# Kernel optimization log

Hardware: AMD Instinct MI355X
Metric: run time of the kernel (lower is better)

The kernel has to match this reference:

```python
import jax, jax.numpy as jnp
import numpy as np
from math import sqrt

DIM = 2048
N_HEADS = 2
HEAD_DIM = DIM // N_HEADS  # 1024 == RoPE dims (dim // 2)
ROPE_DIMS = DIM // 2
ROPE_BASE = 10000.0


def apply_rope(x, dims=ROPE_DIMS, base=ROPE_BASE, offset=0):
    # x: [B, H, L, Dh]; non-traditional (split-half) RoPE over sequence axis
    L = x.shape[-2]
    pos = jnp.arange(offset, offset + L, dtype=x.dtype)[:, None]          # [L,1]
    inv = jnp.exp(jnp.arange(0, dims, 2, dtype=x.dtype) * (-np.log(base) / dims))  # [dims//2]
    theta = pos * inv                                                      # [L, dims//2]
    cos, sin = jnp.cos(theta), jnp.sin(theta)
    h = dims // 2
    x1, x2 = x[..., :h], x[..., h:dims]
    rx1 = x1 * cos - x2 * sin
    rx2 = x1 * sin + x2 * cos
    if dims < x.shape[-1]:
        return jnp.concatenate([rx1, rx2, x[..., dims:]], axis=-1)
    return jnp.concatenate([rx1, rx2], axis=-1)


def setup_inputs() -> dict:
    key = jax.random.key(0)
    ks = jax.random.split(key, 6)
    B, L = 4, 2048
    x = jax.random.normal(ks[0], (B, L, DIM), dtype=jnp.float32)
    # causal additive mask
    causal = jnp.tril(jnp.ones((L, L), dtype=bool))
    mask = jnp.where(causal, 0.0, -1e9).astype(jnp.float32)
    s1 = 1.0 / sqrt(DIM)
    Wqkv_w = jax.random.normal(ks[1], (3 * DIM, DIM), dtype=jnp.float32) * s1
    Wqkv_b = jnp.zeros((3 * DIM,), dtype=jnp.float32)
    out_w = jax.random.normal(ks[2], (DIM, DIM), dtype=jnp.float32) * s1
    out_b = jnp.zeros((DIM,), dtype=jnp.float32)
    return {"x": x, "mask": mask, "Wqkv_w": Wqkv_w, "Wqkv_b": Wqkv_b,
            "out_w": out_w, "out_b": out_b}


def reference(x, mask, Wqkv_w, Wqkv_b, out_w, out_b):
    B, L, D = x.shape
    H, Dh = N_HEADS, HEAD_DIM
    qkv = x @ Wqkv_w.T + Wqkv_b                       # [B, L, 3D]
    q, k, v = jnp.split(qkv, 3, axis=-1)
    # b l (h d) -> b h l d
    split = lambda t: t.reshape(B, L, H, Dh).transpose(0, 2, 1, 3)
    q, k, v = split(q), split(k), split(v)
    q = apply_rope(q)
    k = apply_rope(k)
    scale = sqrt(1.0 / Dh)
    scores = jnp.einsum('bhld,bhkd->bhlk', q * scale, k)  # [B,H,L,L]
    scores = scores + mask                                 # additive causal mask
    probs = jax.nn.softmax(scores, axis=-1)
    vh = jnp.einsum('bhlk,bhkd->bhld', probs, v)
    vh = vh.transpose(0, 2, 1, 3).reshape(B, L, D)         # b h l d -> b l (h d)
    out = vh @ out_w.T + out_b
    return (out, k, v)
```

## Files before the change

### kernel.cpp

```cpp
#include <hip/hip_runtime.h>
#include <hip/hip_bf16.h>
#include <math.h>

typedef unsigned short u16;
typedef __attribute__((ext_vector_type(8))) __bf16 bf16x8;
typedef __attribute__((ext_vector_type(4))) float f32x4;

__device__ __forceinline__ u16 f2b(float f) {
  unsigned u = __builtin_bit_cast(unsigned, f);
  u += 0x7fffu + ((u >> 16) & 1u);
  return (u16)(u >> 16);
}
__device__ __forceinline__ float b2f(u16 h) {
  unsigned u = ((unsigned)h) << 16;
  return __builtin_bit_cast(float, u);
}

__device__ __forceinline__ void gld_lds16(const u16* g, u16* l) {
  __builtin_amdgcn_global_load_lds(
      (const __attribute__((address_space(1))) unsigned int*)g,
      (__attribute__((address_space(3))) unsigned int*)l, 16, 0, 0);
}

template <class FC>
__device__ __forceinline__ void gemm128_body(const u16* A, int lda,
                                             const u16* B, int ldb, FC fc,
                                             int m0, int n0, int K) {
  __shared__ __align__(16) u16 As[128 * 64];
  __shared__ __align__(16) u16 Bs[128 * 64];
  const int tid = threadIdx.x;
  const int wave = tid >> 6;
  const int lane = tid & 63;
  const int srow = lane >> 3;
  const int scol = ((lane & 7) ^ srow) * 8;
  const int wm = (wave & 1) * 64;
  const int wn = (wave >> 1) * 64;
  const int fm = lane & 15;
  const int fs = fm & 7;

  const u16* Abase = A + (size_t)m0 * lda;
  const u16* Bbase = B + (size_t)n0 * ldb;
  const size_t aLane = (size_t)(wave * 8 + srow) * lda + scol;
  const size_t bLane = (size_t)(wave * 8 + srow) * ldb + scol;

  f32x4 acc[4][4];
#pragma unroll
  for (int i = 0; i < 4; ++i)
#pragma unroll
    for (int j = 0; j < 4; ++j) acc[i][j] = (f32x4){0.f, 0.f, 0.f, 0.f};

  for (int k0 = 0; k0 < K; k0 += 64) {
#pragma unroll
    for (int c = 0; c < 4; ++c) {
      gld_lds16(Abase + (aLane + (size_t)(c * 32) * lda + k0),
                &As[(c * 4 + wave) * 512]);
      gld_lds16(Bbase + (bLane + (size_t)(c * 32) * ldb + k0),
                &Bs[(c * 4 + wave) * 512]);
    }
    __syncthreads();
#pragma unroll
    for (int kk = 0; kk < 2; ++kk) {
      const int cb = kk * 4 + (lane >> 4);
      const int p8 = (cb ^ fs) * 8;
      bf16x8 af[4], bfr[4];
#pragma unroll
      for (int i = 0; i < 4; ++i)
        af[i] = *(const bf16x8*)&As[(wm + i * 16 + fm) * 64 + p8];
#pragma unroll
      for (int j = 0; j < 4; ++j)
        bfr[j] = *(const bf16x8*)&Bs[(wn + j * 16 + fm) * 64 + p8];
#pragma unroll
      for (int i = 0; i < 4; ++i)
#pragma unroll
        for (int j = 0; j < 4; ++j)
          acc[i][j] = __builtin_amdgcn_mfma_f32_16x16x32_bf16(
              af[i], bfr[j], acc[i][j], 0, 0, 0);
    }
    __syncthreads();
  }
  const int er = lane >> 4;
#pragma unroll
  for (int i = 0; i < 4; ++i)
#pragma unroll
    for (int j = 0; j < 4; ++j)
#pragma unroll
      for (int r = 0; r < 4; ++r) {
        int m = m0 + wm + i * 16 + er * 4 + r;
        int n = n0 + wn + j * 16 + fm;
        fc(m, n, acc[i][j][r]);
      }
}

struct EQKV {
  u16* qb;
  u16* kb;
  float* vout;
  const float* bias;
  __device__ __forceinline__ void operator()(int m, int n, float v) const {
    v += bias[n];
    int b = m >> 11, l = m & 2047;
    int part = n >> 11, nn = n & 2047, h = nn >> 10, d = nn & 1023;
    size_t idx = ((size_t)((b << 1) + h) * 2048 + l) * 1024 + d;
    if (part == 0)
      qb[idx] = f2b(v);
    else if (part == 1)
      kb[idx] = f2b(v);
    else
      vout[idx] = v;
  }
};
struct EScoreB {
  u16* S;
  __device__ __forceinline__ void operator()(int m, int n, float v) const {
    S[((size_t)m << 11) + n] = f2b(v * 0.03125f + (n > m ? -1.0e9f : 0.0f));
  }
};
struct EBf16 {
  u16* o;
  int ld;
  __device__ __forceinline__ void operator()(int m, int n, float v) const {
    o[(size_t)m * ld + n] = f2b(v);
  }
};
struct EOut {
  float* o;
  const float* bias;
  __device__ __forceinline__ void operator()(int m, int n, float v) const {
    o[((size_t)m << 11) + n] = v + bias[n];
  }
};

__device__ __forceinline__ u16* spz(u16* sp0, u16* sp1, int z) {
  return (z < 4) ? sp0 + (size_t)z * 4194304 : sp1 + (size_t)(z - 4) * 4194304;
}

__global__ void __launch_bounds__(256) k_cast3(const float* x, const float* w1,
                                               const float* w2, u16* xb,
                                               u16* w1b, u16* w2b) {
  long i = (long)(blockIdx.x * 256 + threadIdx.x) * 4;
  const float* src;
  u16* dst;
  long off;
  if (i < 16777216L) {
    src = x; dst = xb; off = i;
  } else if (i < 16777216L + 12582912L) {
    src = w1; dst = w1b; off = i - 16777216L;
  } else {
    src = w2; dst = w2b; off = i - 16777216L - 12582912L;
  }
  float4 f = *(const float4*)(src + off);
  ushort4 o;
  o.x = f2b(f.x);
  o.y = f2b(f.y);
  o.z = f2b(f.z);
  o.w = f2b(f.w);
  *(ushort4*)(dst + off) = o;
}

__global__ void __launch_bounds__(256) k_qkv(const u16* xb, const u16* wb,
                                             const float* bias, u16* qb,
                                             u16* kb, float* vout) {
  gemm128_body(xb, 2048, wb, 2048, EQKV{qb, kb, vout, bias}, blockIdx.y * 128,
               blockIdx.x * 128, 2048);
}

__global__ void __launch_bounds__(256) k_rope(u16* qb, u16* kb, float* kout) {
  int l = blockIdx.x;
  int t = threadIdx.x;
  float lf = (float)l;
  const float c0 = (float)(-9.210340371976184 / 1024.0);
  float s0, c_0, s1, c_1;
  {
    float inv = __expf((float)(2 * t) * c0);
    __sincosf(lf * inv, &s0, &c_0);
    float inv2 = __expf((float)(2 * (t + 256)) * c0);
    __sincosf(lf * inv2, &s1, &c_1);
  }
#pragma unroll
  for (int bh = 0; bh < 8; ++bh) {
    size_t base = ((size_t)bh * 2048 + l) * 1024;
#pragma unroll
    for (int half = 0; half < 2; ++half) {
      int i = t + half * 256;
      float c = half ? c_1 : c_0;
      float s = half ? s1 : s0;
      float x1 = b2f(qb[base + i]), x2 = b2f(qb[base + 512 + i]);
      qb[base + i] = f2b(x1 * c - x2 * s);
      qb[base + 512 + i] = f2b(x1 * s + x2 * c);
      float y1 = b2f(kb[base + i]), y2 = b2f(kb[base + 512 + i]);
      float r1 = y1 * c - y2 * s, r2 = y1 * s + y2 * c;
      kb[base + i] = f2b(r1);
      kb[base + 512 + i] = f2b(r2);
      kout[base + i] = r1;
      kout[base + 512 + i] = r2;
    }
  }
}

__global__ void __launch_bounds__(256) k_transpose_v(const float* v, u16* vt) {
  __shared__ u16 tile[64][65];
  int bh = blockIdx.z;
  int d0 = blockIdx.x * 64, l0 = blockIdx.y * 64;
  const float* vb = v + (size_t)bh * 2048 * 1024;
  u16* vtb = vt + (size_t)bh * 1024 * 2048;
  int t = threadIdx.x;
  int c = t & 63, r4 = t >> 6;
#pragma unroll
  for (int r = 0; r < 16; ++r) {
    int row = r * 4 + r4;
    tile[row][c] = f2b(vb[(size_t)(l0 + row) * 1024 + d0 + c]);
  }
  __syncthreads();
#pragma unroll
  for (int r = 0; r < 16; ++r) {
    int drow = r * 4 + r4;
    vtb[(size_t)(d0 + drow) * 2048 + l0 + c] = tile[c][drow];
  }
}

__global__ void __launch_bounds__(256) k_score(const u16* qb, const u16* kb,
                                               u16* sp0, u16* sp1) {
  int m0 = blockIdx.y * 128, n0 = blockIdx.x * 128;
  if (n0 > m0) return;
  int z = blockIdx.z;
  const u16* q = qb + (size_t)z * 2048 * 1024;
  const u16* k = kb + (size_t)z * 2048 * 1024;
  gemm128_body(q, 1024, k, 1024, EScoreB{spz(sp0, sp1, z)}, m0, n0, 1024);
}

__global__ void __launch_bounds__(256) k_softmax(u16* sp0, u16* sp1) {
  int l = blockIdx.x, z = blockIdx.y;
  u16* row = spz(sp0, sp1, z) + ((size_t)l << 11);
  int t = threadIdx.x;
  int jend = ((l >> 7) + 1) << 7;
  __shared__ float red[4];
  float vals[8];
  float mx = -1e30f;
#pragma unroll
  for (int i = 0; i < 8; ++i) {
    int j = i * 256 + t;
    float v = (j <= l) ? b2f(row[j]) : -1e30f;
    vals[i] = v;
    mx = fmaxf(mx, v);
  }
#pragma unroll
  for (int off = 32; off; off >>= 1) mx = fmaxf(mx, __shfl_down(mx, off));
  if ((t & 63) == 0) red[t >> 6] = mx;
  __syncthreads();
  mx = fmaxf(fmaxf(red[0], red[1]), fmaxf(red[2], red[3]));
  __syncthreads();
  float sum = 0.f;
#pragma unroll
  for (int i = 0; i < 8; ++i) {
    int j = i * 256 + t;
    float e = (j <= l) ? __expf(vals[i] - mx) : 0.f;
    vals[i] = e;
    sum += e;
  }
#pragma unroll
  for (int off = 32; off; off >>= 1) sum += __shfl_down(sum, off);
  if ((t & 63) == 0) red[t >> 6] = sum;
  __syncthreads();
  sum = red[0] + red[1] + red[2] + red[3];
  float is = 1.0f / sum;
#pragma unroll
  for (int i = 0; i < 8; ++i) {
    int j = i * 256 + t;
    if (j < jend) row[j] = f2b(vals[i] * is);
  }
}

__global__ void __launch_bounds__(256) k_pv(u16* sp0, u16* sp1, const u16* vt,
                                            u16* vh) {
  int z = blockIdx.z;
  int b = z >> 1, h = z & 1;
  int m0 = blockIdx.y * 128, n0 = blockIdx.x * 128;
  const u16* Pz = spz(sp0, sp1, z);
  const u16* vtb = vt + (size_t)z * 1024 * 2048;
  u16* outb = vh + (size_t)b * 2048 * 2048 + (size_t)h * 1024;
  int Keff = m0 + 128;
  gemm128_body(Pz, 2048, vtb, 2048, EBf16{outb, 2048}, m0, n0, Keff);
}

__global__ void __launch_bounds__(256) k_out(const u16* vh, const u16* w2,
                                             const float* bias, float* out) {
  gemm128_body(vh, 2048, w2, 2048, EOut{out, bias}, blockIdx.y * 128,
               blockIdx.x * 128, 2048);
}

extern "C" void kernel_launch(void* const* d_in, const int* in_sizes, int n_in,
                              void* d_out, int out_size, void* d_ws,
                              size_t ws_size, hipStream_t stream) {
  const float* x = (const float*)d_in[0];
  const float* w1 = (const float*)d_in[2];
  const float* b1 = (const float*)d_in[3];
  const float* w2 = (const float*)d_in[4];
  const float* b2 = (const float*)d_in[5];
  float* out = (float*)d_out;
  float* kout = out + (size_t)16777216;
  float* vout = kout + (size_t)16777216;

  char* ws = (char*)d_ws;
  u16* xb = (u16*)ws;
  ws += (size_t)33554432;
  u16* w1b = (u16*)ws;
  ws += (size_t)25165824;
  u16* w2b = (u16*)ws;
  ws += (size_t)8388608;
  u16* qb = (u16*)ws;
  ws += (size_t)33554432;
  u16* kb = (u16*)ws;
  ws += (size_t)33554432;
  u16* vtb = (u16*)ws;
  ws += (size_t)33554432;
  u16* sp1 = (u16*)ws;
  u16* sp0 = xb;
  u16* vh = qb;

  k_cast3<<<32768, 256, 0, stream>>>(x, w1, w2, xb, w1b, w2b);
  k_qkv<<<dim3(48, 64), 256, 0, stream>>>(xb, w1b, b1, qb, kb, vout);
  k_rope<<<2048, 256, 0, stream>>>(qb, kb, kout);
  k_transpose_v<<<dim3(16, 32, 8), 256, 0, stream>>>(vout, vtb);
  k_score<<<dim3(16, 16, 8), 256, 0, stream>>>(qb, kb, sp0, sp1);
  k_softmax<<<dim3(2048, 8), 256, 0, stream>>>(sp0, sp1);
  k_pv<<<dim3(8, 16, 8), 256, 0, stream>>>(sp0, sp1, vtb, vh);
  k_out<<<dim3(16, 64), 256, 0, stream>>>(vh, w2b, b2, out);
}
```

Before: 871.9 us.

## Add double-buffered 256x256 GEMM with interleaved prefetch for QKV, PV, out-projection

Introduces a 512-thread, 256x256-tile GEMM body with double-buffered LDS, staged global-to-LDS prefetch interleaved between MFMA phases, barriers and wave priority hints. The QKV, PV and output projection kernels switch to it, and softmax zero-fills up to 256-aligned column boundaries to match the larger PV K extent. The goal is more data reuse per tile and load latency hidden behind MFMA work. It uses 128KB of LDS per block and gives fewer blocks for the smaller GEMMs, which could lower occupancy and hurt tail behaviour.

Result: faster. 807.8 us (-7.3%).

```diff
diff --git a/kernel.cpp b/kernel.cpp
--- a/kernel.cpp
+++ b/kernel.cpp
@@ -21,6 +21,9 @@
       (const __attribute__((address_space(1))) unsigned int*)g,
       (__attribute__((address_space(3))) unsigned int*)l, 16, 0, 0);
 }
+
+#define MFMA16(a, b, c) \
+  c = __builtin_amdgcn_mfma_f32_16x16x32_bf16(a, b, c, 0, 0, 0)
 
 template <class FC>
 __device__ __forceinline__ void gemm128_body(const u16* A, int lda,
@@ -72,9 +75,7 @@
 #pragma unroll
       for (int i = 0; i < 4; ++i)
 #pragma unroll
-        for (int j = 0; j < 4; ++j)
-          acc[i][j] = __builtin_amdgcn_mfma_f32_16x16x32_bf16(
-              af[i], bfr[j], acc[i][j], 0, 0, 0);
+        for (int j = 0; j < 4; ++j) MFMA16(af[i], bfr[j], acc[i][j]);
     }
     __syncthreads();
   }
@@ -89,6 +90,139 @@
         int n = n0 + wn + j * 16 + fm;
         fc(m, n, acc[i][j][r]);
       }
+}
+
+template <class FC>
+__device__ __forceinline__ void gemm256_body(const u16* A, int lda,
+                                             const u16* B, int ldb, FC fc,
+                                             int m0, int n0, int K) {
+  __shared__ __align__(16) u16 As[2][16384];
+  __shared__ __align__(16) u16 Bs[2][16384];
+  const int tid = threadIdx.x;
+  const int wave = tid >> 6;
+  const int lane = tid & 63;
+  const int wr = wave >> 2;
+  const int wc = wave & 3;
+  const int fm = lane & 15;
+  const int cb4 = lane >> 4;
+  const int fs = fm & 7;
+  const int srow = lane >> 3;
+  const int scol = ((lane & 7) ^ srow) * 8;
+
+  const u16* Ab = A + (size_t)(m0 + srow) * lda + scol;
+  const u16* Bb = B + (size_t)(n0 + srow) * ldb + scol;
+
+  const int paRow = (wr * 128 + fm) * 64;
+  const int pbRow = (wc * 64 + fm) * 64;
+  const int q0 = (cb4 ^ fs) * 8;
+  const int q1 = q0 ^ 32;
+
+  f32x4 acc[8][4];
+#pragma unroll
+  for (int m = 0; m < 8; ++m)
+#pragma unroll
+    for (int n = 0; n < 4; ++n) acc[m][n] = (f32x4){0.f, 0.f, 0.f, 0.f};
+
+  auto stA = [&](int bi, int h, int kg) {
+    const u16* g = Ab + (size_t)(h * 128 + wave * 8) * lda + kg;
+    gld_lds16(g, &As[bi][h * 8192 + wave * 512]);
+    gld_lds16(g + (size_t)64 * lda, &As[bi][h * 8192 + (wave + 8) * 512]);
+  };
+  auto stB = [&](int bi, int h, int kg) {
+    const u16* g = Bb + (size_t)(h * 128 + wave * 8) * ldb + kg;
+    gld_lds16(g, &Bs[bi][h * 8192 + wave * 512]);
+    gld_lds16(g + (size_t)64 * ldb, &Bs[bi][h * 8192 + (wave + 8) * 512]);
+  };
+
+  const int nkt = K >> 6;
+
+  stB(0, 0, 0);
+  stB(0, 1, 0);
+  stA(0, 0, 0);
+  stA(0, 1, 0);
+  stB(1, 0, 64);
+  stB(1, 1, 64);
+  stA(1, 0, 64);
+  asm volatile("s_waitcnt vmcnt(6)" ::: "memory");
+  __builtin_amdgcn_s_barrier();
+
+  int buf = 0;
+  for (int T = 0; T < nkt; ++T, buf ^= 1) {
+    const int kc = T * 64;
+    const bool sA1 = (T + 1) < nkt;
+    const bool sN2 = (T + 2) < nkt;
+    bf16x8 af[8], bv[4][2];
+#pragma unroll
+    for (int m = 0; m < 8; ++m)
+      af[m] = *(const bf16x8*)&As[buf][paRow + m * 1024 + q0];
+#pragma unroll
+    for (int n = 0; n < 4; ++n) {
+      bv[n][0] = *(const bf16x8*)&Bs[buf][pbRow + n * 1024 + q0];
+      bv[n][1] = *(const bf16x8*)&Bs[buf][pbRow + n * 1024 + q1];
+    }
+    if (sA1) stA(buf ^ 1, 1, kc + 64);
+    __builtin_amdgcn_s_barrier();
+    asm volatile("s_waitcnt lgkmcnt(0)" ::: "memory");
+    __builtin_amdgcn_sched_barrier(0);
+    __builtin_amdgcn_s_setprio(1);
+#pragma unroll
+    for (int m = 0; m < 8; ++m) {
+      MFMA16(af[m], bv[0][0], acc[m][0]);
+      MFMA16(af[m], bv[1][0], acc[m][1]);
+    }
+    __builtin_amdgcn_s_setprio(0);
+    __builtin_amdgcn_s_barrier();
+    if (sN2) stB(buf, 0, kc + 128);
+    __builtin_amdgcn_s_barrier();
+    __builtin_amdgcn_s_setprio(1);
+#pragma unroll
+    for (int m = 0; m < 8; ++m) {
+      MFMA16(af[m], bv[2][0], acc[m][2]);
+      MFMA16(af[m], bv[3][0], acc[m][3]);
+    }
+    __builtin_amdgcn_s_setprio(0);
+    __builtin_amdgcn_s_barrier();
+#pragma unroll
+    for (int m = 0; m < 8; ++m)
+      af[m] = *(const bf16x8*)&As[buf][paRow + m * 1024 + q1];
+    if (sN2) stB(buf, 1, kc + 128);
+    __builtin_amdgcn_s_barrier();
+    asm volatile("s_waitcnt lgkmcnt(0)" ::: "memory");
+    __builtin_amdgcn_sched_barrier(0);
+    __builtin_amdgcn_s_setprio(1);
+#pragma unroll
+    for (int m = 0; m < 8; ++m) {
+      MFMA16(af[m], bv[0][1], acc[m][0]);
+      MFMA16(af[m], bv[1][1], acc[m][1]);
+    }
+    __builtin_amdgcn_s_setprio(0);
+    __builtin_amdgcn_s_barrier();
+    if (sN2) stA(buf, 0, kc + 128);
+    __builtin_amdgcn_s_barrier();
+    __builtin_amdgcn_s_setprio(1);
+#pragma unroll
+    for (int m = 0; m < 8; ++m) {
+      MFMA16(af[m], bv[2][1], acc[m][2]);
+      MFMA16(af[m], bv[3][1], acc[m][3]);
+    }
+    __builtin_amdgcn_s_setprio(0);
+    if (sN2) {
+      asm volatile("s_waitcnt vmcnt(6)" ::: "memory");
+    } else if (sA1) {
+      asm volatile("s_waitcnt vmcnt(0)" ::: "memory");
+    }
+    __builtin_amdgcn_s_barrier();
+  }
+
+  const int er = lane >> 4;
+#pragma unroll
+  for (int m = 0; m < 8; ++m)
+#pragma unroll
+    for (int n = 0; n < 4; ++n)
+#pragma unroll
+      for (int r = 0; r < 4; ++r)
+        fc(m0 + wr * 128 + m * 16 + er * 4 + r, n0 + wc * 64 + n * 16 + fm,
+           acc[m][n][r]);
 }
 
 struct EQKV {
@@ -157,11 +291,11 @@
   *(ushort4*)(dst + off) = o;
 }
 
-__global__ void __launch_bounds__(256) k_qkv(const u16* xb, const u16* wb,
-                                             const float* bias, u16* qb,
-                                             u16* kb, float* vout) {
-  gemm128_body(xb, 2048, wb, 2048, EQKV{qb, kb, vout, bias}, blockIdx.y * 128,
-               blockIdx.x * 128, 2048);
+__global__ void __launch_bounds__(512, 2) k_qkv(const u16* xb, const u16* wb,
+                                                const float* bias, u16* qb,
+                                                u16* kb, float* vout) {
+  gemm256_body(xb, 2048, wb, 2048, EQKV{qb, kb, vout, bias}, blockIdx.y * 256,
+               blockIdx.x * 256, 2048);
 }
 
 __global__ void __launch_bounds__(256) k_rope(u16* qb, u16* kb, float* kout) {
@@ -232,7 +366,7 @@
   int l = blockIdx.x, z = blockIdx.y;
   u16* row = spz(sp0, sp1, z) + ((size_t)l << 11);
   int t = threadIdx.x;
-  int jend = ((l >> 7) + 1) << 7;
+  int jend = ((l >> 8) + 1) << 8;
   __shared__ float red[4];
   float vals[8];
   float mx = -1e30f;
@@ -270,22 +404,22 @@
   }
 }
 
-__global__ void __launch_bounds__(256) k_pv(u16* sp0, u16* sp1, const u16* vt,
-                                            u16* vh) {
+__global__ void __launch_bounds__(512, 2) k_pv(u16* sp0, u16* sp1,
+                                               const u16* vt, u16* vh) {
   int z = blockIdx.z;
   int b = z >> 1, h = z & 1;
-  int m0 = blockIdx.y * 128, n0 = blockIdx.x * 128;
+  int m0 = blockIdx.y * 256, n0 = blockIdx.x * 256;
   const u16* Pz = spz(sp0, sp1, z);
   const u16* vtb = vt + (size_t)z * 1024 * 2048;
   u16* outb = vh + (size_t)b * 2048 * 2048 + (size_t)h * 1024;
-  int Keff = m0 + 128;
-  gemm128_body(Pz, 2048, vtb, 2048, EBf16{outb, 2048}, m0, n0, Keff);
-}
-
-__global__ void __launch_bounds__(256) k_out(const u16* vh, const u16* w2,
-                                             const float* bias, float* out) {
-  gemm128_body(vh, 2048, w2, 2048, EOut{out, bias}, blockIdx.y * 128,
-               blockIdx.x * 128, 2048);
+  int Keff = m0 + 256;
+  gemm256_body(Pz, 2048, vtb, 2048, EBf16{outb, 2048}, m0, n0, Keff);
+}
+
+__global__ void __launch_bounds__(512, 2) k_out(const u16* vh, const u16* w2,
+                                                const float* bias, float* out) {
+  gemm256_body(vh, 2048, w2, 2048, EOut{out, bias}, blockIdx.y * 256,
+               blockIdx.x * 256, 2048);
 }
 
 extern "C" void kernel_launch(void* const* d_in, const int* in_sizes, int n_in,
@@ -318,11 +452,11 @@
   u16* vh = qb;
 
   k_cast3<<<32768, 256, 0, stream>>>(x, w1, w2, xb, w1b, w2b);
-  k_qkv<<<dim3(48, 64), 256, 0, stream>>>(xb, w1b, b1, qb, kb, vout);
+  k_qkv<<<dim3(24, 32), 512, 0, stream>>>(xb, w1b, b1, qb, kb, vout);
   k_rope<<<2048, 256, 0, stream>>>(qb, kb, kout);
   k_transpose_v<<<dim3(16, 32, 8), 256, 0, stream>>>(vout, vtb);
   k_score<<<dim3(16, 16, 8), 256, 0, stream>>>(qb, kb, sp0, sp1);
   k_softmax<<<dim3(2048, 8), 256, 0, stream>>>(sp0, sp1);
-  k_pv<<<dim3(8, 16, 8), 256, 0, stream>>>(sp0, sp1, vtb, vh);
-  k_out<<<dim3(16, 64), 256, 0, stream>>>(vh, w2b, b2, out);
-}
+  k_pv<<<dim3(4, 8, 8), 512, 0, stream>>>(sp0, sp1, vtb, vh);
+  k_out<<<dim3(8, 32), 512, 0, stream>>>(vh, w2b, b2, out);
+}
```
